# Optimization experiments

Hardware: AMD Instinct MI355X
Metric: run time of the kernel (lower is better)

Reference implementation:

```python
import jax, jax.numpy as jnp
import numpy as np

H = 16  # num_heads
D = 64  # head_dim (latent_dim // num_heads)


def setup_inputs() -> dict:
    key = jax.random.key(0)
    ks = jax.random.split(key, 14)
    B, L, S = 2, 1024, 4096
    input_dim, latent_dim, latent_rank = 2048, 1024, 128
    sc = 0.02
    return {
        "latent": jax.random.normal(ks[0], (B, L, latent_dim), jnp.float32),
        "x": jax.random.normal(ks[1], (B, S, input_dim), jnp.float32),
        "Wq": jax.random.normal(ks[2], (latent_dim, latent_dim), jnp.float32) * sc,
        "bq": jnp.zeros((latent_dim,), jnp.float32),
        "Wc": jax.random.normal(ks[3], (input_dim, latent_rank), jnp.float32) * sc,
        "bc": jnp.zeros((latent_rank,), jnp.float32),
        "Wk": jax.random.normal(ks[4], (latent_rank, latent_dim), jnp.float32) * sc,
        "bk": jnp.zeros((latent_dim,), jnp.float32),
        "Wv": jax.random.normal(ks[5], (latent_rank, latent_dim), jnp.float32) * sc,
        "bv": jnp.zeros((latent_dim,), jnp.float32),
        "Wo": jax.random.normal(ks[6], (latent_dim, latent_dim), jnp.float32) * sc,
        "bo": jnp.zeros((latent_dim,), jnp.float32),
    }


def reference(latent, x, Wq, bq, Wc, bc, Wk, bk, Wv, bv, Wo, bo):
    B, L, latent_dim = latent.shape
    S = x.shape[1]
    # projections
    Q = latent @ Wq + bq                      # [B, L, latent_dim]
    compressed = x @ Wc + bc                  # [B, S, latent_rank] low-rank latent
    K_full = compressed @ Wk + bk             # [B, S, latent_dim]
    V_full = compressed @ Wv + bv             # [B, S, latent_dim]
    # split heads -> [B, H, len, D]
    Qh = Q.reshape(B, L, H, D).transpose(0, 2, 1, 3)
    Kh = K_full.reshape(B, S, H, D).transpose(0, 2, 1, 3)
    Vh = V_full.reshape(B, S, H, D).transpose(0, 2, 1, 3)
    scale = 1.0 / jnp.sqrt(jnp.float32(D))
    scores = jnp.einsum("bhld,bhsd->bhls", Qh, Kh) * scale  # [B,H,L,S]
    attn = jax.nn.softmax(scores, axis=-1)
    ctx = jnp.einsum("bhls,bhsd->bhld", attn, Vh)            # [B,H,L,D]
    ctx = ctx.transpose(0, 2, 1, 3).reshape(B, L, latent_dim)
    return ctx @ Wo + bo
```

## Files before the change

kernel.cpp:

```cpp
#include <hip/hip_runtime.h>
#include <hip/hip_bf16.h>

using bf16x8  = __attribute__((ext_vector_type(8))) short;
using ushort8 = __attribute__((ext_vector_type(8))) unsigned short;
using f32x4   = __attribute__((ext_vector_type(4))) float;

#define DEVINL __device__ __forceinline__

DEVINL unsigned short f2bf(float f) {
    unsigned u = __builtin_bit_cast(unsigned, f);
    u += 0x7FFFu + ((u >> 16) & 1u);
    return (unsigned short)(u >> 16);
}

DEVINL void gload_lds16(const void* g, void* l) {
    __builtin_amdgcn_global_load_lds(
        (const __attribute__((address_space(1))) void*)g,
        (__attribute__((address_space(3))) void*)l, 16, 0, 0);
}

__global__ __launch_bounds__(256) void k_conv(const float* __restrict__ a,
                                              unsigned short* __restrict__ oa, int n8a,
                                              const float* __restrict__ bsrc,
                                              unsigned short* __restrict__ ob, int n8b) {
    int i = blockIdx.x * 256 + threadIdx.x;
    const float* src;
    unsigned short* dst;
    if (i < n8a) { src = a + (size_t)i * 8; dst = oa + (size_t)i * 8; }
    else {
        int j = i - n8a;
        if (j >= n8b) return;
        src = bsrc + (size_t)j * 8; dst = ob + (size_t)j * 8;
    }
    float4 A = *(const float4*)src, B = *(const float4*)(src + 4);
    ushort8 r;
    r[0] = f2bf(A.x); r[1] = f2bf(A.y); r[2] = f2bf(A.z); r[3] = f2bf(A.w);
    r[4] = f2bf(B.x); r[5] = f2bf(B.y); r[6] = f2bf(B.z); r[7] = f2bf(B.w);
    *(ushort8*)dst = r;
}

__global__ __launch_bounds__(256) void k_convT(const float* __restrict__ i0,
                                               unsigned short* __restrict__ o0,
                                               const float* __restrict__ i1,
                                               unsigned short* __restrict__ o1,
                                               int R, int C) {
    __shared__ float t[32][33];
    const float* in = blockIdx.z ? i1 : i0;
    unsigned short* out = blockIdx.z ? o1 : o0;
    int c0 = blockIdx.x * 32, r0 = blockIdx.y * 32;
    int tx = threadIdx.x, ty = threadIdx.y;
#pragma unroll
    for (int i = 0; i < 4; i++)
        t[ty + i * 8][tx] = in[(size_t)(r0 + ty + i * 8) * C + c0 + tx];
    __syncthreads();
#pragma unroll
    for (int i = 0; i < 4; i++)
        out[(size_t)(c0 + ty + i * 8) * R + r0 + tx] = f2bf(t[tx][ty + i * 8]);
}

template <int BM, int BN, int OUTBF, int BIASROW>
__global__ __launch_bounds__(256) void k_gemm(const unsigned short* __restrict__ A,
                                              const unsigned short* __restrict__ BT,
                                              const float* __restrict__ bias,
                                              void* __restrict__ Cout,
                                              int M, int N, int K, float scale,
                                              size_t zA, size_t zB, size_t zC) {
    constexpr int WM = BM / 2, WN = BN / 2, MI = WM / 16, NI = WN / 16;
    constexpr int CA = BM * 8 / 256, CB = BN * 8 / 256;
    __shared__ unsigned short ls[2][(BM + BN) * 64];
    const int tid = threadIdx.x, lane = tid & 63, w = tid >> 6;
    const int m0 = blockIdx.y * BM, n0 = blockIdx.x * BN, zz = blockIdx.z;
    const int mw = (w >> 1) * WM, nw = (w & 1) * WN;
    const int r16 = lane & 15, g4 = lane >> 4;
    A += zA * zz; BT += zB * zz;

    f32x4 acc[MI][NI];
#pragma unroll
    for (int a = 0; a < MI; a++)
#pragma unroll
        for (int b = 0; b < NI; b++) acc[a][b] = (f32x4){0.f, 0.f, 0.f, 0.f};

    auto STAGE = [&](int bufi, int k0) {
        unsigned short* lsA = ls[bufi];
        unsigned short* lsB = ls[bufi] + BM * 64;
#pragma unroll
        for (int i = 0; i < CA; i++) {
            int ch = i * 256 + w * 64 + lane;
            int row = ch >> 3, c = ch & 7;
            gload_lds16(A + (size_t)(m0 + row) * K + k0 + c * 8,
                        lsA + (size_t)(i * 256 + w * 64) * 8);
        }
#pragma unroll
        for (int i = 0; i < CB; i++) {
            int ch = i * 256 + w * 64 + lane;
            int row = ch >> 3, c = ch & 7;
            gload_lds16(BT + (size_t)(n0 + row) * K + k0 + c * 8,
                        lsB + (size_t)(i * 256 + w * 64) * 8);
        }
    };
    auto COMPUTE = [&](int bufi) {
        const unsigned short* lsA = ls[bufi];
        const unsigned short* lsB = ls[bufi] + BM * 64;
#pragma unroll
        for (int kk = 0; kk < 2; kk++) {
            bf16x8 af[MI], bfr[NI];
#pragma unroll
            for (int a = 0; a < MI; a++)
                af[a] = *(const bf16x8*)&lsA[(mw + a * 16 + r16) * 64 + kk * 32 + g4 * 8];
#pragma unroll
            for (int b = 0; b < NI; b++)
                bfr[b] = *(const bf16x8*)&lsB[(nw + b * 16 + r16) * 64 + kk * 32 + g4 * 8];
#pragma unroll
            for (int a = 0; a < MI; a++)
#pragma unroll
                for (int b = 0; b < NI; b++)
                    acc[a][b] = __builtin_amdgcn_mfma_f32_16x16x32_bf16(af[a], bfr[b], acc[a][b], 0, 0, 0);
        }
    };

    const int nk = K >> 6;
    STAGE(0, 0);
    __syncthreads();
    for (int t = 0; t < nk; ++t) {
        if (t + 1 < nk) STAGE((t + 1) & 1, (t + 1) << 6);
        COMPUTE(t & 1);
        __syncthreads();
    }

#pragma unroll
    for (int b = 0; b < NI; b++) {
        int col = n0 + nw + b * 16 + r16;
        float bvc = BIASROW ? 0.f : bias[col];
#pragma unroll
        for (int a = 0; a < MI; a++) {
#pragma unroll
            for (int r = 0; r < 4; r++) {
                int row = m0 + mw + a * 16 + g4 * 4 + r;
                float bv = BIASROW ? bias[row] : bvc;
                float v = (acc[a][b][r] + bv) * scale;
                if (OUTBF)
                    ((unsigned short*)Cout)[zC * zz + (size_t)row * N + col] = f2bf(v);
                else
                    ((float*)Cout)[zC * zz + (size_t)row * N + col] = v;
            }
        }
    }
}

__global__ __launch_bounds__(256, 4) void k_attn(const unsigned short* __restrict__ Qb,
                                                 const unsigned short* __restrict__ Kb,
                                                 const unsigned short* __restrict__ VTb,
                                                 float* __restrict__ ctxp,
                                                 float2* __restrict__ ML) {
    constexpr int LD = 1024;
    __shared__ unsigned short lsK[2][64 * 64];
    __shared__ unsigned short lsVT[2][64 * 64];
    __shared__ unsigned short lsP[4][16 * 64];
    const int tid = threadIdx.x, lane = tid & 63, w = tid >> 6;
    const int r16 = lane & 15, g4 = lane >> 4;
    const int wg = blockIdx.x;
    const int xcd = wg & 7, t_ = wg >> 3, qi = t_ & 15, gg = t_ >> 4;
    const int g = gg * 8 + xcd;
    const int bh = g & 31, z = g >> 5;
    const int b = bh >> 4, h = bh & 15;
    const int q0 = qi * 64 + w * 16;

    const size_t qbase = ((size_t)b * 1024 + q0 + r16) * LD + h * 64;
    bf16x8 qa0 = *(const bf16x8*)&Qb[qbase + g4 * 8];
    bf16x8 qa1 = *(const bf16x8*)&Qb[qbase + 32 + g4 * 8];

    f32x4 ctxa[4];
#pragma unroll
    for (int d = 0; d < 4; d++) ctxa[d] = (f32x4){0.f, 0.f, 0.f, 0.f};
    float m_run = -1e30f, l_run = 0.f;

    const int s7 = r16 & 7;
    const int offk0 = r16 * 64 + ((g4 ^ s7) << 3);
    const int offk1 = r16 * 64 + (((g4 + 4) ^ s7) << 3);
    const int pwb = r16 * 64 + (g4 & 1) * 4;
    const int c2 = g4 >> 1;
    const int swn0 = ((0 + c2) ^ s7) << 3, swn1 = ((2 + c2) ^ s7) << 3;
    const int swn2 = ((4 + c2) ^ s7) << 3, swn3 = ((6 + c2) ^ s7) << 3;

    const int lrow = lane >> 3, lcol = lane & 7;
    const int csrc = lcol ^ lrow;
    const unsigned short* gK = Kb + (size_t)b * 4096 * LD + h * 64 +
                               (size_t)(w * 8 + lrow) * LD + csrc * 8;
    const unsigned short* gV = VTb + (size_t)bh * 64 * 4096 +
                               (size_t)(w * 8 + lrow) * 4096 + csrc * 8;

    auto STAGE = [&](int bufi, int s0) {
        gload_lds16(gK + (size_t)s0 * LD, &lsK[bufi][(w * 8) * 64]);
        gload_lds16(gK + (size_t)(s0 + 32) * LD, &lsK[bufi][(32 + w * 8) * 64]);
        gload_lds16(gV + s0, &lsVT[bufi][(w * 8) * 64]);
        gload_lds16(gV + s0 + 32 * 4096, &lsVT[bufi][(32 + w * 8) * 64]);
    };

    auto COMPUTE = [&](int bufi) {
        f32x4 sc[4];
#pragma unroll
        for (int ni = 0; ni < 4; ni++) sc[ni] = (f32x4){0.f, 0.f, 0.f, 0.f};
        __builtin_amdgcn_s_setprio(1);
#pragma unroll
        for (int kk = 0; kk < 2; kk++) {
            bf16x8 qa = kk ? qa1 : qa0;
            int ofk = kk ? offk1 : offk0;
#pragma unroll
            for (int ni = 0; ni < 4; ni++) {
                bf16x8 kf = *(const bf16x8*)&lsK[bufi][ni * 1024 + ofk];
                sc[ni] = __builtin_amdgcn_mfma_f32_16x16x32_bf16(kf, qa, sc[ni], 0, 0, 0);
            }
        }
        __builtin_amdgcn_s_setprio(0);

        float pmax = sc[0][0];
#pragma unroll
        for (int ni = 0; ni < 4; ni++)
#pragma unroll
            for (int r = 0; r < 4; r++)
                if (ni || r) pmax = fmaxf(pmax, sc[ni][r]);
        pmax = fmaxf(pmax, __shfl_xor(pmax, 16));
        pmax = fmaxf(pmax, __shfl_xor(pmax, 32));

        if (!__all(pmax <= m_run + 8.f)) {
            float mn = fmaxf(m_run, pmax);
            float corr = exp2f(m_run - mn);
            m_run = mn;
            l_run *= corr;
            float c4[4];
#pragma unroll
            for (int r = 0; r < 4; r++) c4[r] = __shfl(corr, g4 * 4 + r);
#pragma unroll
            for (int di = 0; di < 4; di++)
#pragma unroll
                for (int r = 0; r < 4; r++) ctxa[di][r] *= c4[r];
        }

        float p[4][4];
        float rs = 0.f;
#pragma unroll
        for (int ni = 0; ni < 4; ni++)
#pragma unroll
            for (int r = 0; r < 4; r++) {
                p[ni][r] = exp2f(sc[ni][r] - m_run);
                rs += p[ni][r];
            }
        rs += __shfl_xor(rs, 16);
        rs += __shfl_xor(rs, 32);
        l_run += rs;

#pragma unroll
        for (int ni = 0; ni < 4; ni++) {
            int sw = ni == 0 ? swn0 : ni == 1 ? swn1 : ni == 2 ? swn2 : swn3;
            unsigned u0, u1;
            asm("v_cvt_pk_bf16_f32 %0, %1, %2" : "=v"(u0) : "v"(p[ni][0]), "v"(p[ni][1]));
            asm("v_cvt_pk_bf16_f32 %0, %1, %2" : "=v"(u1) : "v"(p[ni][2]), "v"(p[ni][3]));
            *(uint2*)&lsP[w][pwb + sw] = make_uint2(u0, u1);
        }

        __builtin_amdgcn_s_setprio(1);
#pragma unroll
        for (int kk = 0; kk < 2; kk++) {
            int ofk = kk ? offk1 : offk0;
            bf16x8 pa = *(const bf16x8*)&lsP[w][ofk];
#pragma unroll
            for (int di = 0; di < 4; di++) {
                bf16x8 vf = *(const bf16x8*)&lsVT[bufi][di * 1024 + ofk];
                ctxa[di] = __builtin_amdgcn_mfma_f32_16x16x32_bf16(pa, vf, ctxa[di], 0, 0, 0);
            }
        }
        __builtin_amdgcn_s_setprio(0);
    };

    const int t0 = (z * 64) / 3, t1 = ((z + 1) * 64) / 3;
    STAGE(0, t0 * 64);
    __syncthreads();
#pragma unroll 1
    for (int t = t0; t < t1; ++t) {
        int pb = (t - t0) & 1;
        if (t + 1 < t1) STAGE(pb ^ 1, (t + 1) * 64);
        COMPUTE(pb);
        __syncthreads();
    }

    float* cp = ctxp + ((size_t)z * 2 + b) * 1024 * 1024;
#pragma unroll
    for (int r = 0; r < 4; r++) {
        int q = q0 + g4 * 4 + r;
#pragma unroll
        for (int di = 0; di < 4; di++)
            cp[(size_t)q * 1024 + h * 64 + di * 16 + r16] = ctxa[di][r];
    }
    if (g4 == 0)
        ML[(((size_t)z * 2 + b) * 16 + h) * 1024 + q0 + r16] = make_float2(m_run, l_run);
}

__global__ __launch_bounds__(256) void k_merge(const float* __restrict__ ctxp,
                                               const float2* __restrict__ ML,
                                               unsigned short* __restrict__ ctx) {
    int gid = blockIdx.x * 256 + threadIdx.x;
    int d8 = gid & 7, h = (gid >> 3) & 15, q = (gid >> 7) & 1023, b = gid >> 17;
    float m[3], l[3];
#pragma unroll
    for (int z = 0; z < 3; z++) {
        float2 e = ML[(((size_t)z * 2 + b) * 16 + h) * 1024 + q];
        m[z] = e.x; l[z] = e.y;
    }
    float M = fmaxf(fmaxf(m[0], m[1]), m[2]);
    float wz[3], L = 0.f;
#pragma unroll
    for (int z = 0; z < 3; z++) { wz[z] = exp2f(m[z] - M); L += wz[z] * l[z]; }
    float inv = 1.0f / L;
    float o[8];
#pragma unroll
    for (int j = 0; j < 8; j++) o[j] = 0.f;
#pragma unroll
    for (int z = 0; z < 3; z++) {
        const float4* p = (const float4*)(ctxp + ((size_t)z * 2 + b) * 1048576 +
                                          (size_t)q * 1024 + h * 64 + d8 * 8);
        float4 a = p[0], c = p[1];
        o[0] += wz[z] * a.x; o[1] += wz[z] * a.y; o[2] += wz[z] * a.z; o[3] += wz[z] * a.w;
        o[4] += wz[z] * c.x; o[5] += wz[z] * c.y; o[6] += wz[z] * c.z; o[7] += wz[z] * c.w;
    }
    ushort8 r;
#pragma unroll
    for (int j = 0; j < 8; j++) r[j] = f2bf(o[j] * inv);
    *(ushort8*)&ctx[((size_t)b * 1024 + q) * 1024 + h * 64 + d8 * 8] = r;
}

extern "C" void kernel_launch(void* const* d_in, const int* in_sizes, int n_in,
                              void* d_out, int out_size, void* d_ws, size_t ws_size,
                              hipStream_t stream) {
    const float* latent = (const float*)d_in[0];
    const float* x      = (const float*)d_in[1];
    const float* Wq     = (const float*)d_in[2];
    const float* bq     = (const float*)d_in[3];
    const float* Wc     = (const float*)d_in[4];
    const float* bc     = (const float*)d_in[5];
    const float* Wk     = (const float*)d_in[6];
    const float* bk     = (const float*)d_in[7];
    const float* Wv     = (const float*)d_in[8];
    const float* bv     = (const float*)d_in[9];
    const float* Wo     = (const float*)d_in[10];
    const float* bo     = (const float*)d_in[11];
    float* out = (float*)d_out;

    char* ws = (char*)d_ws;
    size_t off = 0;
    auto alloc = [&](size_t shorts) {
        void* p = ws + off;
        off += (shorts * 2 + 255) & ~(size_t)255;
        return (unsigned short*)p;
    };
    unsigned short* lat_bf = alloc(2097152);
    unsigned short* x_bf   = alloc(16777216);
    unsigned short* WqT    = alloc(1048576);
    unsigned short* WcT    = alloc(262144);
    unsigned short* WkT    = alloc(131072);
    unsigned short* WvT    = alloc(131072);
    unsigned short* WoT    = alloc(1048576);
    unsigned short* comp   = alloc(1048576);
    unsigned short* Qb     = alloc(2097152);
    unsigned short* Kb     = alloc(8388608);
    unsigned short* VTb    = alloc(8388608);
    unsigned short* ctxb   = alloc(2097152);
    float*          ctxp   = (float*)alloc(12582912);
    float2*         MLp    = (float2*)alloc(393216);

    dim3 tb(32, 8);
    k_conv<<<9216, 256, 0, stream>>>(latent, lat_bf, 262144, x, x_bf, 2097152);
    k_convT<<<dim3(32, 32, 2), tb, 0, stream>>>(Wq, WqT, Wo, WoT, 1024, 1024);
    k_convT<<<dim3(32, 4, 2), tb, 0, stream>>>(Wk, WkT, Wv, WvT, 128, 1024);
    k_convT<<<dim3(4, 64, 1), tb, 0, stream>>>(Wc, WcT, Wc, WcT, 2048, 128);

    k_gemm<32, 128, 1, 0><<<dim3(1, 256, 1), 256, 0, stream>>>(
        x_bf, WcT, bc, comp, 8192, 128, 2048, 1.f, 0, 0, 0);
    k_gemm<64, 64, 1, 0><<<dim3(16, 32, 1), 256, 0, stream>>>(
        lat_bf, WqT, bq, Qb, 2048, 1024, 1024, 0.18033688f, 0, 0, 0);
    k_gemm<128, 128, 1, 0><<<dim3(8, 64, 1), 256, 0, stream>>>(
        comp, WkT, bk, Kb, 8192, 1024, 128, 1.f, 0, 0, 0);
    k_gemm<64, 64, 1, 1><<<dim3(64, 16, 2), 256, 0, stream>>>(
        WvT, comp, bv, VTb, 1024, 4096, 128, 1.f,
        0, (size_t)4096 * 128, (size_t)16 * 64 * 4096);
    k_attn<<<1536, 256, 0, stream>>>(Qb, Kb, VTb, ctxp, MLp);
    k_merge<<<1024, 256, 0, stream>>>(ctxp, MLp, ctxb);
    k_gemm<64, 64, 0, 0><<<dim3(16, 32, 1), 256, 0, stream>>>(
        ctxb, WoT, bo, out, 2048, 1024, 1024, 1.f, 0, 0, 0);
}
```

Before: 284.1 us.

## Fuse fp32-to-bf16 conversion and split-KV merge into GEMM A-operand loading

```diff
diff --git a/kernel.cpp b/kernel.cpp
--- a/kernel.cpp
+++ b/kernel.cpp
@@ -17,26 +17,6 @@
     __builtin_amdgcn_global_load_lds(
         (const __attribute__((address_space(1))) void*)g,
         (__attribute__((address_space(3))) void*)l, 16, 0, 0);
-}
-
-__global__ __launch_bounds__(256) void k_conv(const float* __restrict__ a,
-                                              unsigned short* __restrict__ oa, int n8a,
-                                              const float* __restrict__ bsrc,
-                                              unsigned short* __restrict__ ob, int n8b) {
-    int i = blockIdx.x * 256 + threadIdx.x;
-    const float* src;
-    unsigned short* dst;
-    if (i < n8a) { src = a + (size_t)i * 8; dst = oa + (size_t)i * 8; }
-    else {
-        int j = i - n8a;
-        if (j >= n8b) return;
-        src = bsrc + (size_t)j * 8; dst = ob + (size_t)j * 8;
-    }
-    float4 A = *(const float4*)src, B = *(const float4*)(src + 4);
-    ushort8 r;
-    r[0] = f2bf(A.x); r[1] = f2bf(A.y); r[2] = f2bf(A.z); r[3] = f2bf(A.w);
-    r[4] = f2bf(B.x); r[5] = f2bf(B.y); r[6] = f2bf(B.z); r[7] = f2bf(B.w);
-    *(ushort8*)dst = r;
 }
 
 __global__ __launch_bounds__(256) void k_convT(const float* __restrict__ i0,
@@ -58,21 +38,32 @@
         out[(size_t)(c0 + ty + i * 8) * R + r0 + tx] = f2bf(t[tx][ty + i * 8]);
 }
 
-template <int BM, int BN, int OUTBF, int BIASROW>
-__global__ __launch_bounds__(256) void k_gemm(const unsigned short* __restrict__ A,
+template <int BM, int BN, int OUTBF, int BIASROW, int AMODE>
+__global__ __launch_bounds__(256) void k_gemm(const void* __restrict__ Ain,
                                               const unsigned short* __restrict__ BT,
                                               const float* __restrict__ bias,
                                               void* __restrict__ Cout,
                                               int M, int N, int K, float scale,
-                                              size_t zA, size_t zB, size_t zC) {
+                                              size_t zA, size_t zB, size_t zC,
+                                              const float2* __restrict__ ML) {
     constexpr int WM = BM / 2, WN = BN / 2, MI = WM / 16, NI = WN / 16;
-    constexpr int CA = BM * 8 / 256, CB = BN * 8 / 256;
+    constexpr int CB = BN * 8 / 256;
+    constexpr int CA = BM * 8 / 256;
+    constexpr int EPT = BM * 64 / 256;
+    constexpr int TPR = 64 / EPT;
+    constexpr int NAREG = (AMODE == 2) ? EPT / 2 : (AMODE == 1 ? EPT / 4 : 1);
     __shared__ unsigned short ls[2][(BM + BN) * 64];
     const int tid = threadIdx.x, lane = tid & 63, w = tid >> 6;
     const int m0 = blockIdx.y * BM, n0 = blockIdx.x * BN, zz = blockIdx.z;
     const int mw = (w >> 1) * WM, nw = (w & 1) * WN;
     const int r16 = lane & 15, g4 = lane >> 4;
-    A += zA * zz; BT += zB * zz;
+    const unsigned short* A16 = (const unsigned short*)Ain + zA * zz;
+    const float* A32 = (const float*)Ain;
+    BT += zB * zz;
+    const int arow = tid / TPR, acol = (tid % TPR) * EPT;
+
+    float4 areg[NAREG];
+    float2 mle[2];
 
     f32x4 acc[MI][NI];
 #pragma unroll
@@ -80,16 +71,69 @@
 #pragma unroll
         for (int b = 0; b < NI; b++) acc[a][b] = (f32x4){0.f, 0.f, 0.f, 0.f};
 
-    auto STAGE = [&](int bufi, int k0) {
-        unsigned short* lsA = ls[bufi];
-        unsigned short* lsB = ls[bufi] + BM * 64;
-#pragma unroll
-        for (int i = 0; i < CA; i++) {
-            int ch = i * 256 + w * 64 + lane;
-            int row = ch >> 3, c = ch & 7;
-            gload_lds16(A + (size_t)(m0 + row) * K + k0 + c * 8,
-                        lsA + (size_t)(i * 256 + w * 64) * 8);
-        }
+    auto LOAD_A = [&](int bufi, int k0) {
+        if constexpr (AMODE == 0) {
+#pragma unroll
+            for (int i = 0; i < CA; i++) {
+                int ch = i * 256 + w * 64 + lane;
+                int row = ch >> 3, c = ch & 7;
+                gload_lds16(A16 + (size_t)(m0 + row) * K + k0 + c * 8,
+                            &ls[bufi][(size_t)(i * 256 + w * 64) * 8]);
+            }
+        } else if constexpr (AMODE == 1) {
+            const float* src = A32 + (size_t)(m0 + arow) * K + k0 + acol;
+#pragma unroll
+            for (int j = 0; j < EPT / 4; j++) areg[j] = *(const float4*)(src + j * 4);
+        } else {
+            const float* src = A32 + (size_t)(m0 + arow) * K + k0 + acol;
+#pragma unroll
+            for (int j = 0; j < EPT / 4; j++) {
+                areg[j] = *(const float4*)(src + j * 4);
+                areg[j + EPT / 4] = *(const float4*)(src + 2097152 + j * 4);
+            }
+            int b = (m0 + arow) >> 10, q = (m0 + arow) & 1023, h = k0 >> 6;
+            mle[0] = ML[((size_t)(b * 16 + h)) * 1024 + q];
+            mle[1] = ML[((size_t)((2 + b) * 16 + h)) * 1024 + q];
+        }
+    };
+
+    auto WRITE_A = [&](int bufi) {
+        if constexpr (AMODE == 1) {
+            unsigned u[EPT / 2];
+#pragma unroll
+            for (int j = 0; j < EPT / 4; j++) {
+                asm("v_cvt_pk_bf16_f32 %0, %1, %2"
+                    : "=v"(u[2 * j]) : "v"(areg[j].x), "v"(areg[j].y));
+                asm("v_cvt_pk_bf16_f32 %0, %1, %2"
+                    : "=v"(u[2 * j + 1]) : "v"(areg[j].z), "v"(areg[j].w));
+            }
+#pragma unroll
+            for (int j = 0; j < EPT / 8; j++)
+                *(uint4*)&ls[bufi][arow * 64 + acol + j * 8] =
+                    make_uint4(u[4 * j], u[4 * j + 1], u[4 * j + 2], u[4 * j + 3]);
+        } else if constexpr (AMODE == 2) {
+            float Mx = fmaxf(mle[0].x, mle[1].x);
+            float w0 = exp2f(mle[0].x - Mx), w1 = exp2f(mle[1].x - Mx);
+            float inv = 1.f / (w0 * mle[0].y + w1 * mle[1].y);
+            w0 *= inv; w1 *= inv;
+            unsigned u[EPT / 2];
+#pragma unroll
+            for (int j = 0; j < EPT / 4; j++) {
+                float4 a = areg[j], c = areg[j + EPT / 4];
+                float v0 = w0 * a.x + w1 * c.x, v1 = w0 * a.y + w1 * c.y;
+                float v2 = w0 * a.z + w1 * c.z, v3 = w0 * a.w + w1 * c.w;
+                asm("v_cvt_pk_bf16_f32 %0, %1, %2" : "=v"(u[2 * j]) : "v"(v0), "v"(v1));
+                asm("v_cvt_pk_bf16_f32 %0, %1, %2" : "=v"(u[2 * j + 1]) : "v"(v2), "v"(v3));
+            }
+#pragma unroll
+            for (int j = 0; j < EPT / 8; j++)
+                *(uint4*)&ls[bufi][arow * 64 + acol + j * 8] =
+                    make_uint4(u[4 * j], u[4 * j + 1], u[4 * j + 2], u[4 * j + 3]);
+        }
+    };
+
+    auto STAGE_B = [&](int bufi, int k0) {
+        unsigned short* lsB = &ls[bufi][BM * 64];
 #pragma unroll
         for (int i = 0; i < CB; i++) {
             int ch = i * 256 + w * 64 + lane;
@@ -98,9 +142,10 @@
                         lsB + (size_t)(i * 256 + w * 64) * 8);
         }
     };
+
     auto COMPUTE = [&](int bufi) {
         const unsigned short* lsA = ls[bufi];
-        const unsigned short* lsB = ls[bufi] + BM * 64;
+        const unsigned short* lsB = &ls[bufi][BM * 64];
 #pragma unroll
         for (int kk = 0; kk < 2; kk++) {
             bf16x8 af[MI], bfr[NI];
@@ -119,11 +164,15 @@
     };
 
     const int nk = K >> 6;
-    STAGE(0, 0);
+    LOAD_A(0, 0);
+    STAGE_B(0, 0);
+    if constexpr (AMODE != 0) WRITE_A(0);
     __syncthreads();
     for (int t = 0; t < nk; ++t) {
-        if (t + 1 < nk) STAGE((t + 1) & 1, (t + 1) << 6);
-        COMPUTE(t & 1);
+        int cur = t & 1, nxt = cur ^ 1;
+        if (t + 1 < nk) { LOAD_A(nxt, (t + 1) << 6); STAGE_B(nxt, (t + 1) << 6); }
+        COMPUTE(cur);
+        if (AMODE != 0 && t + 1 < nk) WRITE_A(nxt);
         __syncthreads();
     }
 
@@ -272,7 +321,7 @@
         __builtin_amdgcn_s_setprio(0);
     };
 
-    const int t0 = (z * 64) / 3, t1 = ((z + 1) * 64) / 3;
+    const int t0 = z * 32, t1 = t0 + 32;
     STAGE(0, t0 * 64);
     __syncthreads();
 #pragma unroll 1
@@ -293,39 +342,6 @@
     }
     if (g4 == 0)
         ML[(((size_t)z * 2 + b) * 16 + h) * 1024 + q0 + r16] = make_float2(m_run, l_run);
-}
-
-__global__ __launch_bounds__(256) void k_merge(const float* __restrict__ ctxp,
-                                               const float2* __restrict__ ML,
-                                               unsigned short* __restrict__ ctx) {
-    int gid = blockIdx.x * 256 + threadIdx.x;
-    int d8 = gid & 7, h = (gid >> 3) & 15, q = (gid >> 7) & 1023, b = gid >> 17;
-    float m[3], l[3];
-#pragma unroll
-    for (int z = 0; z < 3; z++) {
-        float2 e = ML[(((size_t)z * 2 + b) * 16 + h) * 1024 + q];
-        m[z] = e.x; l[z] = e.y;
-    }
-    float M = fmaxf(fmaxf(m[0], m[1]), m[2]);
-    float wz[3], L = 0.f;
-#pragma unroll
-    for (int z = 0; z < 3; z++) { wz[z] = exp2f(m[z] - M); L += wz[z] * l[z]; }
-    float inv = 1.0f / L;
-    float o[8];
-#pragma unroll
-    for (int j = 0; j < 8; j++) o[j] = 0.f;
-#pragma unroll
-    for (int z = 0; z < 3; z++) {
-        const float4* p = (const float4*)(ctxp + ((size_t)z * 2 + b) * 1048576 +
-                                          (size_t)q * 1024 + h * 64 + d8 * 8);
-        float4 a = p[0], c = p[1];
-        o[0] += wz[z] * a.x; o[1] += wz[z] * a.y; o[2] += wz[z] * a.z; o[3] += wz[z] * a.w;
-        o[4] += wz[z] * c.x; o[5] += wz[z] * c.y; o[6] += wz[z] * c.z; o[7] += wz[z] * c.w;
-    }
-    ushort8 r;
-#pragma unroll
-    for (int j = 0; j < 8; j++) r[j] = f2bf(o[j] * inv);
-    *(ushort8*)&ctx[((size_t)b * 1024 + q) * 1024 + h * 64 + d8 * 8] = r;
 }
 
 extern "C" void kernel_launch(void* const* d_in, const int* in_sizes, int n_in,
@@ -352,38 +368,33 @@
         off += (shorts * 2 + 255) & ~(size_t)255;
         return (unsigned short*)p;
     };
-    unsigned short* lat_bf = alloc(2097152);
-    unsigned short* x_bf   = alloc(16777216);
-    unsigned short* WqT    = alloc(1048576);
-    unsigned short* WcT    = alloc(262144);
-    unsigned short* WkT    = alloc(131072);
-    unsigned short* WvT    = alloc(131072);
-    unsigned short* WoT    = alloc(1048576);
-    unsigned short* comp   = alloc(1048576);
-    unsigned short* Qb     = alloc(2097152);
-    unsigned short* Kb     = alloc(8388608);
-    unsigned short* VTb    = alloc(8388608);
-    unsigned short* ctxb   = alloc(2097152);
-    float*          ctxp   = (float*)alloc(12582912);
-    float2*         MLp    = (float2*)alloc(393216);
+    unsigned short* WqT  = alloc(1048576);
+    unsigned short* WcT  = alloc(262144);
+    unsigned short* WkT  = alloc(131072);
+    unsigned short* WvT  = alloc(131072);
+    unsigned short* WoT  = alloc(1048576);
+    unsigned short* comp = alloc(1048576);
+    unsigned short* Qb   = alloc(2097152);
+    unsigned short* Kb   = alloc(8388608);
+    unsigned short* VTb  = alloc(8388608);
+    float*          ctxp = (float*)alloc(8388608);
+    float2*         MLp  = (float2*)alloc(262144);
 
     dim3 tb(32, 8);
-    k_conv<<<9216, 256, 0, stream>>>(latent, lat_bf, 262144, x, x_bf, 2097152);
     k_convT<<<dim3(32, 32, 2), tb, 0, stream>>>(Wq, WqT, Wo, WoT, 1024, 1024);
     k_convT<<<dim3(32, 4, 2), tb, 0, stream>>>(Wk, WkT, Wv, WvT, 128, 1024);
     k_convT<<<dim3(4, 64, 1), tb, 0, stream>>>(Wc, WcT, Wc, WcT, 2048, 128);
 
-    k_gemm<32, 128, 1, 0><<<dim3(1, 256, 1), 256, 0, stream>>>(
-        x_bf, WcT, bc, comp, 8192, 128, 2048, 1.f, 0, 0, 0);
-    k_gemm<64, 64, 1, 0><<<dim3(16, 32, 1), 256, 0, stream>>>(
-        lat_bf, WqT, bq, Qb, 2048, 1024, 1024, 0.18033688f, 0, 0, 0);
-    k_gemm<128, 128, 1, 0><<<dim3(8, 64, 1), 256, 0, stream>>>(
-        comp, WkT, bk, Kb, 8192, 1024, 128, 1.f, 0, 0, 0);
-    k_gemm<64, 64, 1, 1><<<dim3(64, 16, 2), 256, 0, stream>>>(
+    k_gemm<32, 128, 1, 0, 1><<<dim3(1, 256, 1), 256, 0, stream>>>(
+        x, WcT, bc, comp, 8192, 128, 2048, 1.f, 0, 0, 0, nullptr);
+    k_gemm<64, 64, 1, 0, 1><<<dim3(16, 32, 1), 256, 0, stream>>>(
+        latent, WqT, bq, Qb, 2048, 1024, 1024, 0.18033688f, 0, 0, 0, nullptr);
+    k_gemm<128, 128, 1, 0, 0><<<dim3(8, 64, 1), 256, 0, stream>>>(
+        comp, WkT, bk, Kb, 8192, 1024, 128, 1.f, 0, 0, 0, nullptr);
+    k_gemm<64, 64, 1, 1, 0><<<dim3(64, 16, 2), 256, 0, stream>>>(
         WvT, comp, bv, VTb, 1024, 4096, 128, 1.f,
-        0, (size_t)4096 * 128, (size_t)16 * 64 * 4096);
-    k_attn<<<1536, 256, 0, stream>>>(Qb, Kb, VTb, ctxp, MLp);
-    k_merge<<<1024, 256, 0, stream>>>(ctxp, MLp, ctxb);
-    k_gemm<64, 64, 0, 0><<<dim3(16, 32, 1), 256, 0, stream>>>(
-        ctxb, WoT, bo, out, 2048, 1024, 1024, 1.f, 0, 0, 0);
-}
+        0, (size_t)4096 * 128, (size_t)16 * 64 * 4096, nullptr);
+    k_attn<<<1024, 256, 0, stream>>>(Qb, Kb, VTb, ctxp, MLp);
+    k_gemm<64, 64, 0, 0, 2><<<dim3(16, 32, 1), 256, 0, stream>>>(
+        ctxp, WoT, bo, out, 2048, 1024, 1024, 1.f, 0, 0, 0, MLp);
+}
```

After: 300.5 us. 1.06x slower.
